# Optimization experiments

Measured on AMD Instinct MI355X. Metric: run time of the kernel, lower is better.

Reference implementation:

```python
import jax, jax.numpy as jnp
import numpy as np
import math

SUB_LEN = 5

def _row_mask(index, sub_len, win_len):
    # Faithful port of logsparseAttention.row_mask (numpy, built at trace time).
    log_l = math.ceil(math.log2(sub_len))
    mask = np.zeros(win_len, dtype=np.float32)
    if (win_len // sub_len) * 2 * log_l > index:
        mask[: index + 1] = 1.0
    else:
        while index >= 0:
            if index - log_l + 1 < 0:
                mask[:index] = 1.0
                break
            mask[index - log_l + 1 : index + 1] = 1.0
            for i in range(log_l):
                new_index = index - log_l + 1 - 2 ** i
                if index - new_index <= sub_len and new_index >= 0:
                    mask[new_index] = 1.0
            index -= sub_len
    return mask

def _log_mask(win_len, sub_len):
    m = np.stack([_row_mask(i, sub_len, win_len) for i in range(win_len)])
    return m[None, None]  # [1, 1, L, L]

def setup_inputs() -> dict:
    key = jax.random.key(0)
    kq, kk, kv = jax.random.split(key, 3)
    B, L, H, D = 4, 2048, 16, 64
    return {
        "queries": jax.random.normal(kq, (B, L, H, D), dtype=jnp.float32),
        "keys": jax.random.normal(kk, (B, L, H, D), dtype=jnp.float32),
        "values": jax.random.normal(kv, (B, L, H, D), dtype=jnp.float32),
        "attn_mask": jnp.zeros((1,), dtype=jnp.int32),  # unused by the module
    }

def reference(queries, keys, values, attn_mask):
    L = queries.shape[1]
    mask = jnp.asarray(_log_mask(L, SUB_LEN), dtype=queries.dtype)  # [1,1,L,L]
    q = jnp.swapaxes(queries, 1, 2)            # [B, H, L, D]
    k = jnp.transpose(keys, (0, 2, 3, 1))      # [B, H, D, L]
    v = jnp.swapaxes(values, 1, 2)             # [B, H, L, D]
    pre_att = jnp.matmul(q, k)                 # [B, H, L, L] (no scaling: scale=None)
    pre_att = pre_att * mask + (-1e9) * (1.0 - mask)
    att = jax.nn.softmax(pre_att, axis=-1)
    return jnp.matmul(att, v)                  # [B, H, L, D]
```

## Files before the change

### kernel.cpp

```cpp
#include <hip/hip_runtime.h>


typedef __attribute__((ext_vector_type(8))) short short8;
typedef __attribute__((ext_vector_type(4))) float floatx4;
typedef _Float16 half8 __attribute__((ext_vector_type(8)));
typedef _Float16 half4 __attribute__((ext_vector_type(4)));

#define NB 4
#define NL 2048
#define NH 16
#define ND 64
#define PADK 72
#define PADQ 72

static __device__ __forceinline__ unsigned short f2bf(float f) {
    unsigned int u = __float_as_uint(f);
    u += 0x7fff + ((u >> 16) & 1);
    return (unsigned short)(u >> 16);
}
static __device__ __forceinline__ float bf2f(unsigned short h) {
    return __uint_as_float(((unsigned int)h) << 16);
}

__global__ __launch_bounds__(256)
void conv_kv(const float* __restrict__ Kg, const float* __restrict__ Vg,
             _Float16* __restrict__ Kf, _Float16* __restrict__ Vt) {
    __shared__ float tile[64][65];
    const int kt = blockIdx.x;
    const int bh = blockIdx.y;
    const int b  = bh >> 4, h = bh & 15;
    const int t  = threadIdx.x;
    const int row = t >> 2;
    const int seg = (t & 3) * 16;
    const size_t gsrc = (((size_t)(b * NL + kt * 64 + row) * NH + h) << 6) + seg;
    {
        float kv[16];
        #pragma unroll
        for (int i = 0; i < 16; i += 4) *(float4*)(kv + i) = *(const float4*)(Kg + gsrc + i);
        half8 o0, o1;
        #pragma unroll
        for (int j2 = 0; j2 < 8; ++j2) { o0[j2] = (_Float16)kv[j2]; o1[j2] = (_Float16)kv[8 + j2]; }
        _Float16* kd = Kf + (((size_t)(bh * NL + kt * 64 + row)) << 6) + seg;
        *(half8*)kd = o0;
        *(half8*)(kd + 8) = o1;
    }
    {
        #pragma unroll
        for (int i = 0; i < 16; i += 4) {
            float4 v = *(const float4*)(Vg + gsrc + i);
            tile[row][seg + i + 0] = v.x;
            tile[row][seg + i + 1] = v.y;
            tile[row][seg + i + 2] = v.z;
            tile[row][seg + i + 3] = v.w;
        }
    }
    __syncthreads();
    #pragma unroll
    for (int pass = 0; pass < 2; ++pass) {
        const int d  = pass * 32 + (t >> 3);
        const int kk = (t & 7) * 8;
        half8 o;
        #pragma unroll
        for (int j2 = 0; j2 < 8; ++j2) o[j2] = (_Float16)tile[kk + j2][d];
        *(half8*)(Vt + (((size_t)(bh * 64 + d)) << 11) + kt * 64 + kk) = o;
    }
}

__global__ __launch_bounds__(512, 4)
void lsattn_main(const float* __restrict__ Qg,
                 const _Float16* __restrict__ Kf,
                 const _Float16* __restrict__ Vt,
                 float* __restrict__ Og) {
    __shared__ alignas(16) _Float16 Ks[64 * PADK];
    __shared__ alignas(16) _Float16 Vs[64 * PADK];
    __shared__ alignas(16) _Float16 Ps[8 * 16 * PADQ];

    const int id   = (int)blockIdx.x;
    const int bh   = id & 63;
    const int pr   = id >> 6;
    const int tid  = threadIdx.x;
    const int lane = tid & 63;
    const int w    = tid >> 6;
    const int col  = lane & 15;
    const int quad = lane >> 4;

    const int sa   = (w < 4) ? pr : (31 - pr);
    const int qrow = sa * 64 + (w & 3) * 16 + col;

    half8 qf[2];
    {
        const float* qp = Qg + (((size_t)((bh >> 4) * NL + qrow) * NH + (bh & 15)) << 6) + quad * 8;
        #pragma unroll
        for (int c = 0; c < 2; ++c) {
            float4 a = *(const float4*)(qp + c * 32);
            float4 b = *(const float4*)(qp + c * 32 + 4);
            qf[c][0] = (_Float16)a.x; qf[c][1] = (_Float16)a.y;
            qf[c][2] = (_Float16)a.z; qf[c][3] = (_Float16)a.w;
            qf[c][4] = (_Float16)b.x; qf[c][5] = (_Float16)b.y;
            qf[c][6] = (_Float16)b.z; qf[c][7] = (_Float16)b.w;
        }
    }

    floatx4 ofrag[4];
    #pragma unroll
    for (int i = 0; i < 4; ++i) ofrag[i] = floatx4{0.f, 0.f, 0.f, 0.f};
    float m_run = -1e30f, l_run = 0.f;

    const int srow = tid >> 3;
    const int sseg = (tid & 7) * 8;
    const _Float16* kgb = Kf + (((size_t)(bh * NL)) << 6) + (srow << 6) + sseg;
    const _Float16* vgb = Vt + (((size_t)bh) << 17) + ((size_t)srow << 11) + sseg;
    _Float16* pbuf = Ps + w * 16 * PADQ;

    const int TB = 31 - pr;

    half8 kpre = *(const half8*)(kgb);
    half8 vpre = *(const half8*)(vgb);

    for (int t = 0; t <= TB; ++t) {
        const int j0 = t * 64;
        __syncthreads();
        *(half8*)(Ks + srow * PADK + sseg) = kpre;
        *(half8*)(Vs + srow * PADK + sseg) = vpre;
        if (t < TB) {
            kpre = *(const half8*)(kgb + (t + 1) * 4096);
            vpre = *(const half8*)(vgb + (t + 1) * 64);
        }
        __syncthreads();

        if (t > sa) continue;

        floatx4 stf[4];
        #pragma unroll
        for (int f = 0; f < 4; ++f) {
            floatx4 acc = floatx4{0.f, 0.f, 0.f, 0.f};
            #pragma unroll
            for (int c = 0; c < 2; ++c) {
                half8 kfr = *(const half8*)(Ks + (f * 16 + col) * PADK + c * 32 + quad * 8);
                acc = __builtin_amdgcn_mfma_f32_16x16x32_f16(kfr, qf[c], acc, 0, 0, 0);
            }
            stf[f] = acc;
        }

        if (t == sa) {
            #pragma unroll
            for (int f = 0; f < 4; ++f)
                #pragma unroll
                for (int r = 0; r < 4; ++r) {
                    const int key = j0 + f * 16 + quad * 4 + r;
                    if (key > qrow) stf[f][r] = -1e30f;
                }
        }

        float mt = -1e30f;
        #pragma unroll
        for (int f = 0; f < 4; ++f)
            #pragma unroll
            for (int r = 0; r < 4; ++r) mt = fmaxf(mt, stf[f][r]);
        mt = fmaxf(mt, __shfl_xor(mt, 16));
        mt = fmaxf(mt, __shfl_xor(mt, 32));
        const float m_new = fmaxf(m_run, mt);
        const float alpha = __expf(m_run - m_new);
        float ls = 0.f;
        #pragma unroll
        for (int f = 0; f < 4; ++f)
            #pragma unroll
            for (int r = 0; r < 4; ++r) {
                const float p = __expf(stf[f][r] - m_new);
                stf[f][r] = p;
                ls += p;
            }
        ls += __shfl_xor(ls, 16);
        ls += __shfl_xor(ls, 32);
        l_run = l_run * alpha + ls;
        m_run = m_new;
        #pragma unroll
        for (int mc = 0; mc < 4; ++mc) ofrag[mc] *= alpha;

        #pragma unroll
        for (int f = 0; f < 4; ++f) {
            half4 hp;
            hp[0] = (_Float16)stf[f][0]; hp[1] = (_Float16)stf[f][1];
            hp[2] = (_Float16)stf[f][2]; hp[3] = (_Float16)stf[f][3];
            *(half4*)(pbuf + col * PADQ + f * 16 + quad * 4) = hp;
        }
        half8 pf0 = *(const half8*)(pbuf + col * PADQ + quad * 8);
        half8 pf1 = *(const half8*)(pbuf + col * PADQ + 32 + quad * 8);

        #pragma unroll
        for (int mc = 0; mc < 4; ++mc) {
            half8 vf0 = *(const half8*)(Vs + (mc * 16 + col) * PADK + quad * 8);
            half8 vf1 = *(const half8*)(Vs + (mc * 16 + col) * PADK + 32 + quad * 8);
            ofrag[mc] = __builtin_amdgcn_mfma_f32_16x16x32_f16(vf0, pf0, ofrag[mc], 0, 0, 0);
            ofrag[mc] = __builtin_amdgcn_mfma_f32_16x16x32_f16(vf1, pf1, ofrag[mc], 0, 0, 0);
        }
    }

    const float inv = 1.f / l_run;
    float* op = Og + ((size_t)bh * NL + qrow) * ND;
    #pragma unroll
    for (int mc = 0; mc < 4; ++mc) {
        float4 o;
        o.x = ofrag[mc][0] * inv;
        o.y = ofrag[mc][1] * inv;
        o.z = ofrag[mc][2] * inv;
        o.w = ofrag[mc][3] * inv;
        *(float4*)(op + mc * 16 + quad * 4) = o;
    }
}

__global__ __launch_bounds__(256)
void lsattn_fb(const float* __restrict__ Qg,
               const float* __restrict__ Kg,
               const float* __restrict__ Vg,
               float* __restrict__ Og) {
    __shared__ alignas(16) unsigned short Kh[64 * PADK];
    __shared__ alignas(16) unsigned short Kl[64 * PADK];
    __shared__ alignas(16) unsigned short Vh[64 * PADK];

    const int qt   = 31 - (int)blockIdx.x;
    const int bh   = blockIdx.y;
    const int tid  = threadIdx.x;
    const int lane = tid & 63;
    const int w    = tid >> 6;
    const int col  = lane & 15;
    const int quad = lane >> 4;
    const int qrow = qt * 64 + w * 16 + col;

    short8 qhi[2], qlo[2];
    {
        const float* qp = Qg + ((bh >> 4) * NL + qrow) * (NH * ND) + (bh & 15) * ND + quad * 8;
        #pragma unroll
        for (int c = 0; c < 2; ++c) {
            float qv[8];
            *(float4*)(qv + 0) = *(const float4*)(qp + c * 32);
            *(float4*)(qv + 4) = *(const float4*)(qp + c * 32 + 4);
            #pragma unroll
            for (int j = 0; j < 8; ++j) {
                unsigned short h = f2bf(qv[j]);
                qhi[c][j] = (short)h;
                qlo[c][j] = (short)f2bf(qv[j] - bf2f(h));
            }
        }
    }
    floatx4 ofrag[4];
    #pragma unroll
    for (int i = 0; i < 4; ++i) ofrag[i] = floatx4{0.f, 0.f, 0.f, 0.f};
    float m_run = -1e30f, l_run = 0.f;
    const int skey  = tid >> 2;
    const int sdb   = (tid & 3) * 16;
    const int gbase = (bh >> 4) * NL * NH * ND + (bh & 15) * ND;

    for (int t = 0; t <= qt; ++t) {
        const int j0 = t * 64;
        __syncthreads();
        {
            const int gro = gbase + (j0 + skey) * (NH * ND) + sdb;
            float kv[16], vv[16];
            #pragma unroll
            for (int i = 0; i < 16; i += 4) {
                *(float4*)(kv + i) = *(const float4*)(Kg + gro + i);
                *(float4*)(vv + i) = *(const float4*)(Vg + gro + i);
            }
            short8 h0, h1, l0, l1;
            #pragma unroll
            for (int j = 0; j < 8; ++j) {
                unsigned short h = f2bf(kv[j]);
                h0[j] = (short)h; l0[j] = (short)f2bf(kv[j] - bf2f(h));
                unsigned short g = f2bf(kv[8 + j]);
                h1[j] = (short)g; l1[j] = (short)f2bf(kv[8 + j] - bf2f(g));
            }
            *(short8*)(Kh + skey * PADK + sdb)     = h0;
            *(short8*)(Kh + skey * PADK + sdb + 8) = h1;
            *(short8*)(Kl + skey * PADK + sdb)     = l0;
            *(short8*)(Kl + skey * PADK + sdb + 8) = l1;
            #pragma unroll
            for (int i = 0; i < 16; ++i) Vh[(sdb + i) * PADK + skey] = f2bf(vv[i]);
        }
        __syncthreads();

        floatx4 stf[4];
        #pragma unroll
        for (int f = 0; f < 4; ++f) {
            floatx4 acc = floatx4{0.f, 0.f, 0.f, 0.f};
            #pragma unroll
            for (int c = 0; c < 2; ++c) {
                short8 kh = *(const short8*)(Kh + (f * 16 + col) * PADK + c * 32 + quad * 8);
                short8 kl = *(const short8*)(Kl + (f * 16 + col) * PADK + c * 32 + quad * 8);
                acc = __builtin_amdgcn_mfma_f32_16x16x32_bf16(kh, qhi[c], acc, 0, 0, 0);
                acc = __builtin_amdgcn_mfma_f32_16x16x32_bf16(kl, qhi[c], acc, 0, 0, 0);
                acc = __builtin_amdgcn_mfma_f32_16x16x32_bf16(kh, qlo[c], acc, 0, 0, 0);
            }
            stf[f] = acc;
        }
        if (t == qt) {
            #pragma unroll
            for (int f = 0; f < 4; ++f)
                #pragma unroll
                for (int r = 0; r < 4; ++r) {
                    const int key = j0 + f * 16 + quad * 4 + r;
                    if (key > qrow) stf[f][r] = -1e30f;
                }
        }
        float mt = -1e30f;
        #pragma unroll
        for (int f = 0; f < 4; ++f)
            #pragma unroll
            for (int r = 0; r < 4; ++r) mt = fmaxf(mt, stf[f][r]);
        mt = fmaxf(mt, __shfl_xor(mt, 16));
        mt = fmaxf(mt, __shfl_xor(mt, 32));
        const float m_new = fmaxf(m_run, mt);
        const float alpha = __expf(m_run - m_new);
        float ls = 0.f;
        #pragma unroll
        for (int f = 0; f < 4; ++f)
            #pragma unroll
            for (int r = 0; r < 4; ++r) {
                const float p = __expf(stf[f][r] - m_new);
                stf[f][r] = p; ls += p;
            }
        ls += __shfl_xor(ls, 16);
        ls += __shfl_xor(ls, 32);
        l_run = l_run * alpha + ls;
        m_run = m_new;
        #pragma unroll
        for (int mc = 0; mc < 4; ++mc) ofrag[mc] *= alpha;

        short8 pfrag[2];
        #pragma unroll
        for (int kc = 0; kc < 2; ++kc) {
            #pragma unroll
            for (int jj = 0; jj < 8; ++jj) {
                const int r  = jj & 3;
                const int sq = (quad & 1) * 2 + (jj >> 2);
                const int sl = col + (sq << 4);
                const float va = __shfl(stf[kc * 2 + 0][r], sl);
                const float vb = __shfl(stf[kc * 2 + 1][r], sl);
                pfrag[kc][jj] = (short)f2bf((quad & 2) ? vb : va);
            }
        }
        #pragma unroll
        for (int mc = 0; mc < 4; ++mc) {
            #pragma unroll
            for (int kc = 0; kc < 2; ++kc) {
                short8 vf = *(const short8*)(Vh + (mc * 16 + col) * PADK + kc * 32 + quad * 8);
                ofrag[mc] = __builtin_amdgcn_mfma_f32_16x16x32_bf16(vf, pfrag[kc], ofrag[mc], 0, 0, 0);
            }
        }
    }
    const float inv = 1.f / l_run;
    float* op = Og + ((size_t)bh * NL + qrow) * ND;
    #pragma unroll
    for (int mc = 0; mc < 4; ++mc) {
        float4 o;
        o.x = ofrag[mc][0] * inv; o.y = ofrag[mc][1] * inv;
        o.z = ofrag[mc][2] * inv; o.w = ofrag[mc][3] * inv;
        *(float4*)(op + mc * 16 + quad * 4) = o;
    }
}

extern "C" void kernel_launch(void* const* d_in, const int* in_sizes, int n_in,
                              void* d_out, int out_size, void* d_ws, size_t ws_size,
                              hipStream_t stream) {
    const float* Q = (const float*)d_in[0];
    const float* K = (const float*)d_in[1];
    const float* V = (const float*)d_in[2];
    float* O = (float*)d_out;

    const size_t elems = (size_t)NB * NL * NH * ND;
    if (ws_size >= 2 * elems * sizeof(_Float16)) {
        _Float16* Kf = (_Float16*)d_ws;
        _Float16* Vt = Kf + elems;
        conv_kv<<<dim3(32, 64), dim3(256), 0, stream>>>(K, V, Kf, Vt);
        lsattn_main<<<dim3(1024), dim3(512), 0, stream>>>(Q, Kf, Vt, O);
    } else {
        lsattn_fb<<<dim3(32, 64), dim3(256), 0, stream>>>(Q, K, V, O);
    }
}
```

Baseline: 197.9 us.

## Process four 16-row query chunks per wave to reuse K/V fragments

Each wave now handles 64 query rows (four 16-row chunks) instead of 16. K and V fragments are loaded from shared memory into registers once per tile and reused across the four chunks. Blocks shrink to 256 threads, and the grid is halved to 512 blocks with 128-row paired query tiles for causal load balancing. This cuts LDS read traffic and block count, but raises register pressure (ofrag 4x4, qf 4x2, kfr/vfr), which may lower occupancy, and leaves fewer blocks to cover the GPU.

Result: slower. 215.7 us (+9.0%).

```diff
diff --git a/kernel.cpp b/kernel.cpp
--- a/kernel.cpp
+++ b/kernel.cpp
@@ -66,14 +66,14 @@
     }
 }
 
-__global__ __launch_bounds__(512, 4)
+__global__ __launch_bounds__(256, 2)
 void lsattn_main(const float* __restrict__ Qg,
                  const _Float16* __restrict__ Kf,
                  const _Float16* __restrict__ Vt,
                  float* __restrict__ Og) {
     __shared__ alignas(16) _Float16 Ks[64 * PADK];
     __shared__ alignas(16) _Float16 Vs[64 * PADK];
-    __shared__ alignas(16) _Float16 Ps[8 * 16 * PADQ];
+    __shared__ alignas(16) _Float16 Ps[4 * 16 * PADQ];
 
     const int id   = (int)blockIdx.x;
     const int bh   = id & 63;
@@ -84,128 +84,152 @@
     const int col  = lane & 15;
     const int quad = lane >> 4;
 
-    const int sa   = (w < 4) ? pr : (31 - pr);
-    const int qrow = sa * 64 + (w & 3) * 16 + col;
-
-    half8 qf[2];
-    {
-        const float* qp = Qg + (((size_t)((bh >> 4) * NL + qrow) * NH + (bh & 15)) << 6) + quad * 8;
+    const int base128 = (w < 2) ? pr : (15 - pr);
+    const int qbase   = base128 * 128 + (w & 1) * 64;
+    const int sa      = qbase >> 6;
+
+    half8 qf[4][2];
+    #pragma unroll
+    for (int qc = 0; qc < 4; ++qc) {
+        const float* qp = Qg + (((size_t)((bh >> 4) * NL + qbase + qc * 16 + col) * NH + (bh & 15)) << 6) + quad * 8;
         #pragma unroll
         for (int c = 0; c < 2; ++c) {
             float4 a = *(const float4*)(qp + c * 32);
             float4 b = *(const float4*)(qp + c * 32 + 4);
-            qf[c][0] = (_Float16)a.x; qf[c][1] = (_Float16)a.y;
-            qf[c][2] = (_Float16)a.z; qf[c][3] = (_Float16)a.w;
-            qf[c][4] = (_Float16)b.x; qf[c][5] = (_Float16)b.y;
-            qf[c][6] = (_Float16)b.z; qf[c][7] = (_Float16)b.w;
-        }
-    }
-
-    floatx4 ofrag[4];
-    #pragma unroll
-    for (int i = 0; i < 4; ++i) ofrag[i] = floatx4{0.f, 0.f, 0.f, 0.f};
-    float m_run = -1e30f, l_run = 0.f;
-
-    const int srow = tid >> 3;
-    const int sseg = (tid & 7) * 8;
+            qf[qc][c][0] = (_Float16)a.x; qf[qc][c][1] = (_Float16)a.y;
+            qf[qc][c][2] = (_Float16)a.z; qf[qc][c][3] = (_Float16)a.w;
+            qf[qc][c][4] = (_Float16)b.x; qf[qc][c][5] = (_Float16)b.y;
+            qf[qc][c][6] = (_Float16)b.z; qf[qc][c][7] = (_Float16)b.w;
+        }
+    }
+
+    floatx4 ofrag[4][4];
+    #pragma unroll
+    for (int qc = 0; qc < 4; ++qc)
+        #pragma unroll
+        for (int mc = 0; mc < 4; ++mc) ofrag[qc][mc] = floatx4{0.f, 0.f, 0.f, 0.f};
+    float m_run[4] = {-1e30f, -1e30f, -1e30f, -1e30f};
+    float l_run[4] = {0.f, 0.f, 0.f, 0.f};
+
+    const int srow = tid >> 2;
+    const int sseg = (tid & 3) * 16;
     const _Float16* kgb = Kf + (((size_t)(bh * NL)) << 6) + (srow << 6) + sseg;
     const _Float16* vgb = Vt + (((size_t)bh) << 17) + ((size_t)srow << 11) + sseg;
     _Float16* pbuf = Ps + w * 16 * PADQ;
 
-    const int TB = 31 - pr;
-
-    half8 kpre = *(const half8*)(kgb);
-    half8 vpre = *(const half8*)(vgb);
+    const int TB = 31 - 2 * pr;
+
+    half8 kpre0 = *(const half8*)(kgb);
+    half8 kpre1 = *(const half8*)(kgb + 8);
+    half8 vpre0 = *(const half8*)(vgb);
+    half8 vpre1 = *(const half8*)(vgb + 8);
 
     for (int t = 0; t <= TB; ++t) {
         const int j0 = t * 64;
         __syncthreads();
-        *(half8*)(Ks + srow * PADK + sseg) = kpre;
-        *(half8*)(Vs + srow * PADK + sseg) = vpre;
+        *(half8*)(Ks + srow * PADK + sseg)     = kpre0;
+        *(half8*)(Ks + srow * PADK + sseg + 8) = kpre1;
+        *(half8*)(Vs + srow * PADK + sseg)     = vpre0;
+        *(half8*)(Vs + srow * PADK + sseg + 8) = vpre1;
         if (t < TB) {
-            kpre = *(const half8*)(kgb + (t + 1) * 4096);
-            vpre = *(const half8*)(vgb + (t + 1) * 64);
+            kpre0 = *(const half8*)(kgb + (t + 1) * 4096);
+            kpre1 = *(const half8*)(kgb + (t + 1) * 4096 + 8);
+            vpre0 = *(const half8*)(vgb + (t + 1) * 64);
+            vpre1 = *(const half8*)(vgb + (t + 1) * 64 + 8);
         }
         __syncthreads();
 
         if (t > sa) continue;
 
-        floatx4 stf[4];
+        half8 kfr[4][2], vfr[4][2];
         #pragma unroll
         for (int f = 0; f < 4; ++f) {
-            floatx4 acc = floatx4{0.f, 0.f, 0.f, 0.f};
-            #pragma unroll
-            for (int c = 0; c < 2; ++c) {
-                half8 kfr = *(const half8*)(Ks + (f * 16 + col) * PADK + c * 32 + quad * 8);
-                acc = __builtin_amdgcn_mfma_f32_16x16x32_f16(kfr, qf[c], acc, 0, 0, 0);
-            }
-            stf[f] = acc;
-        }
-
-        if (t == sa) {
+            kfr[f][0] = *(const half8*)(Ks + (f * 16 + col) * PADK + quad * 8);
+            kfr[f][1] = *(const half8*)(Ks + (f * 16 + col) * PADK + 32 + quad * 8);
+            vfr[f][0] = *(const half8*)(Vs + (f * 16 + col) * PADK + quad * 8);
+            vfr[f][1] = *(const half8*)(Vs + (f * 16 + col) * PADK + 32 + quad * 8);
+        }
+
+        const bool diag = (t == sa);
+        #pragma unroll
+        for (int qc = 0; qc < 4; ++qc) {
+            const int qrow = qbase + qc * 16 + col;
+
+            floatx4 stf[4];
+            #pragma unroll
+            for (int f = 0; f < 4; ++f) {
+                floatx4 acc = floatx4{0.f, 0.f, 0.f, 0.f};
+                acc = __builtin_amdgcn_mfma_f32_16x16x32_f16(kfr[f][0], qf[qc][0], acc, 0, 0, 0);
+                acc = __builtin_amdgcn_mfma_f32_16x16x32_f16(kfr[f][1], qf[qc][1], acc, 0, 0, 0);
+                stf[f] = acc;
+            }
+
+            if (diag) {
+                #pragma unroll
+                for (int f = 0; f < 4; ++f)
+                    #pragma unroll
+                    for (int r = 0; r < 4; ++r) {
+                        const int key = j0 + f * 16 + quad * 4 + r;
+                        if (key > qrow) stf[f][r] = -1e30f;
+                    }
+            }
+
+            float mt = -1e30f;
+            #pragma unroll
+            for (int f = 0; f < 4; ++f)
+                #pragma unroll
+                for (int r = 0; r < 4; ++r) mt = fmaxf(mt, stf[f][r]);
+            mt = fmaxf(mt, __shfl_xor(mt, 16));
+            mt = fmaxf(mt, __shfl_xor(mt, 32));
+            const float m_new = fmaxf(m_run[qc], mt);
+            const float alpha = __expf(m_run[qc] - m_new);
+            float ls = 0.f;
             #pragma unroll
             for (int f = 0; f < 4; ++f)
                 #pragma unroll
                 for (int r = 0; r < 4; ++r) {
-                    const int key = j0 + f * 16 + quad * 4 + r;
-                    if (key > qrow) stf[f][r] = -1e30f;
+                    const float p = __expf(stf[f][r] - m_new);
+                    stf[f][r] = p;
+                    ls += p;
                 }
-        }
-
-        float mt = -1e30f;
-        #pragma unroll
-        for (int f = 0; f < 4; ++f)
-            #pragma unroll
-            for (int r = 0; r < 4; ++r) mt = fmaxf(mt, stf[f][r]);
-        mt = fmaxf(mt, __shfl_xor(mt, 16));
-        mt = fmaxf(mt, __shfl_xor(mt, 32));
-        const float m_new = fmaxf(m_run, mt);
-        const float alpha = __expf(m_run - m_new);
-        float ls = 0.f;
-        #pragma unroll
-        for (int f = 0; f < 4; ++f)
-            #pragma unroll
-            for (int r = 0; r < 4; ++r) {
-                const float p = __expf(stf[f][r] - m_new);
-                stf[f][r] = p;
-                ls += p;
-            }
-        ls += __shfl_xor(ls, 16);
-        ls += __shfl_xor(ls, 32);
-        l_run = l_run * alpha + ls;
-        m_run = m_new;
-        #pragma unroll
-        for (int mc = 0; mc < 4; ++mc) ofrag[mc] *= alpha;
-
-        #pragma unroll
-        for (int f = 0; f < 4; ++f) {
-            half4 hp;
-            hp[0] = (_Float16)stf[f][0]; hp[1] = (_Float16)stf[f][1];
-            hp[2] = (_Float16)stf[f][2]; hp[3] = (_Float16)stf[f][3];
-            *(half4*)(pbuf + col * PADQ + f * 16 + quad * 4) = hp;
-        }
-        half8 pf0 = *(const half8*)(pbuf + col * PADQ + quad * 8);
-        half8 pf1 = *(const half8*)(pbuf + col * PADQ + 32 + quad * 8);
-
+            ls += __shfl_xor(ls, 16);
+            ls += __shfl_xor(ls, 32);
+            l_run[qc] = l_run[qc] * alpha + ls;
+            m_run[qc] = m_new;
+            #pragma unroll
+            for (int mc = 0; mc < 4; ++mc) ofrag[qc][mc] *= alpha;
+
+            #pragma unroll
+            for (int f = 0; f < 4; ++f) {
+                half4 hp;
+                hp[0] = (_Float16)stf[f][0]; hp[1] = (_Float16)stf[f][1];
+                hp[2] = (_Float16)stf[f][2]; hp[3] = (_Float16)stf[f][3];
+                *(half4*)(pbuf + col * PADQ + f * 16 + quad * 4) = hp;
+            }
+            half8 pf0 = *(const half8*)(pbuf + col * PADQ + quad * 8);
+            half8 pf1 = *(const half8*)(pbuf + col * PADQ + 32 + quad * 8);
+
+            #pragma unroll
+            for (int mc = 0; mc < 4; ++mc) {
+                ofrag[qc][mc] = __builtin_amdgcn_mfma_f32_16x16x32_f16(vfr[mc][0], pf0, ofrag[qc][mc], 0, 0, 0);
+                ofrag[qc][mc] = __builtin_amdgcn_mfma_f32_16x16x32_f16(vfr[mc][1], pf1, ofrag[qc][mc], 0, 0, 0);
+            }
+        }
+    }
+
+    #pragma unroll
+    for (int qc = 0; qc < 4; ++qc) {
+        const float inv = 1.f / l_run[qc];
+        float* op = Og + ((size_t)bh * NL + qbase + qc * 16 + col) * ND;
         #pragma unroll
         for (int mc = 0; mc < 4; ++mc) {
-            half8 vf0 = *(const half8*)(Vs + (mc * 16 + col) * PADK + quad * 8);
-            half8 vf1 = *(const half8*)(Vs + (mc * 16 + col) * PADK + 32 + quad * 8);
-            ofrag[mc] = __builtin_amdgcn_mfma_f32_16x16x32_f16(vf0, pf0, ofrag[mc], 0, 0, 0);
-            ofrag[mc] = __builtin_amdgcn_mfma_f32_16x16x32_f16(vf1, pf1, ofrag[mc], 0, 0, 0);
-        }
-    }
-
-    const float inv = 1.f / l_run;
-    float* op = Og + ((size_t)bh * NL + qrow) * ND;
-    #pragma unroll
-    for (int mc = 0; mc < 4; ++mc) {
-        float4 o;
-        o.x = ofrag[mc][0] * inv;
-        o.y = ofrag[mc][1] * inv;
-        o.z = ofrag[mc][2] * inv;
-        o.w = ofrag[mc][3] * inv;
-        *(float4*)(op + mc * 16 + quad * 4) = o;
+            float4 o;
+            o.x = ofrag[qc][mc][0] * inv;
+            o.y = ofrag[qc][mc][1] * inv;
+            o.z = ofrag[qc][mc][2] * inv;
+            o.w = ofrag[qc][mc][3] * inv;
+            *(float4*)(op + mc * 16 + quad * 4) = o;
+        }
     }
 }
 
@@ -372,7 +396,7 @@
         _Float16* Kf = (_Float16*)d_ws;
         _Float16* Vt = Kf + elems;
         conv_kv<<<dim3(32, 64), dim3(256), 0, stream>>>(K, V, Kf, Vt);
-        lsattn_main<<<dim3(1024), dim3(512), 0, stream>>>(Q, Kf, Vt, O);
+        lsattn_main<<<dim3(512), dim3(256), 0, stream>>>(Q, Kf, Vt, O);
     } else {
         lsattn_fb<<<dim3(32, 64), dim3(256), 0, stream>>>(Q, K, V, O);
     }
```
